# Kernel optimization log

Hardware: AMD Instinct MI355X
Metric: run time of the kernel (lower is better)

Reference implementation:

```python
import jax, jax.numpy as jnp
import numpy as np

B, N, S, K = 16, 4096, 1024, 32
DIN, DINC, DOUT = 64, 67, 64
MAX_VALUE = 1e10


def setup_inputs() -> dict:
    key = jax.random.key(0)
    ks = jax.random.split(key, 6)
    x = jax.random.normal(ks[0], (B, N, DIN), dtype=jnp.float32)
    x_complete = jax.random.normal(ks[1], (B, N, DINC), dtype=jnp.float32)
    # neighbor indices in [-1, N); -1 denotes padding (masked out in pooling)
    indexes = jax.random.randint(ks[2], (B, S, K), -1, N, dtype=jnp.int64)
    # first neighbor is the center point and must be valid
    indexes = indexes.at[:, :, 0].set(jnp.abs(indexes[:, :, 0]) % N)
    weight1 = jax.random.normal(ks[3], (DOUT, DINC), dtype=jnp.float32) * 0.05
    weight2 = jax.random.normal(ks[4], (DOUT, DIN), dtype=jnp.float32) * 0.05
    bias = jax.random.normal(ks[5], (DOUT,), dtype=jnp.float32) * 0.05
    return {"x": x, "x_complete": x_complete, "indexes": indexes,
            "weight1": weight1, "weight2": weight2, "bias": bias, "use_x": 1}


def reference(x, x_complete, indexes, weight1, weight2, bias, use_x):
    # pooling_operation = 'max' (hardcoded; string arg in original module)
    Bq, Nq, _ = x.shape
    _, Sq, Kq = indexes.shape
    C = weight1.shape[0]
    # dense linear projections
    xc = jnp.einsum('bnd,cd->bnc', x_complete, weight1) + bias  # (B,N,C)
    xp = jnp.einsum('bnd,cd->bnc', x, weight2)                  # (B,N,C)
    if use_x:
        xc = xc + xp
    # prepend a zero row so index -1 (-> slot 0) gathers zeros
    pad = jnp.concatenate([jnp.zeros((Bq, 1, C), xc.dtype), xc], axis=1)  # (B,N+1,C)
    idx1 = indexes + 1                                          # (B,S,K)
    g = jnp.take_along_axis(pad, idx1.reshape(Bq, Sq * Kq, 1), axis=1)
    g = g.reshape(Bq, Sq, Kq, C)                                # (B,S,K,C)
    if use_x:
        if Nq == Sq:
            g = g - xp[:, :, None, :]
        else:
            xp_pad = jnp.concatenate([jnp.zeros((Bq, 1, C), xp.dtype), xp], axis=1)
            center = jnp.take_along_axis(xp_pad, (indexes[:, :, 0] + 1)[:, :, None], axis=1)  # (B,S,C)
            g = g - center[:, :, None, :]
    # masked max over the neighbor axis: padded slots pushed to -MAX_VALUE
    mask = (idx1 == 0).astype(g.dtype)[..., None]               # (B,S,K,1)
    out = jnp.max(g - MAX_VALUE * mask, axis=2)                 # (B,S,C)
    return out
```

## Files before the change

### kernel.cpp

```cpp
#include <hip/hip_runtime.h>

#define B_    16
#define N_    4096
#define S_    1024
#define K_    32
#define DIN_  64
#define DINC_ 67
#define DOUT_ 64
#define ROWS_ (B_ * N_)
#define NCH   128
#define NFRAG 2560
#define ASTR  168

typedef float f32x4 __attribute__((ext_vector_type(4)));
typedef short s16x8 __attribute__((ext_vector_type(8)));

static __device__ __forceinline__ unsigned short f2bf(float f) {
    unsigned int u = __float_as_uint(f);
    u = (u + 0x7fffu + ((u >> 16) & 1u)) >> 16;
    return (unsigned short)u;
}
static __device__ __forceinline__ float bf2f(unsigned short h) {
    return __uint_as_float((unsigned int)h << 16);
}

__global__ __launch_bounds__(256) void prep_kernel(
    const float* __restrict__ w1, const float* __restrict__ w2,
    const int* __restrict__ use_x_p, uint4* __restrict__ wf)
{
    const int id = blockIdx.x * 256 + threadIdx.x;
    if (id >= NFRAG) return;
    const int s  = id >> 9;
    const int nt = (id >> 6) & 7;
    const int l  = id & 63;
    const int q  = l >> 4, m = l & 15;
    const int c  = nt * 16 + m;
    const int ux = use_x_p[0];

    unsigned int w[4];
#pragma unroll
    for (int p = 0; p < 4; ++p) {
        unsigned short h[2];
#pragma unroll
        for (int e = 0; e < 2; ++e) {
            const int j = p * 2 + e;
            const int k = s * 32 + q * 8 + j;
            float v = 0.f;
            if (c < 64) {
                if (k < DINC_)      v = w1[c * DINC_ + k];
                else if (k < 131)   v = ux ? w2[c * DIN_ + (k - DINC_)] : 0.f;
            } else {
                if (k >= DINC_ && k < 131) v = w2[(c - 64) * DIN_ + (k - DINC_)];
            }
            h[e] = f2bf(v);
        }
        w[p] = (unsigned int)h[0] | ((unsigned int)h[1] << 16);
    }
    wf[id] = make_uint4(w[0], w[1], w[2], w[3]);
}

__global__ __launch_bounds__(256) void proj_kernel(
    const float* __restrict__ x, const float* __restrict__ xcm,
    const uint4* __restrict__ wf, const float* __restrict__ bias,
    unsigned short* __restrict__ cmb)
{
    __shared__ uint4 ldsb[NFRAG];
    __shared__ unsigned short lact[64 * ASTR];

    const int t    = threadIdx.x;
    const int row0 = (blockIdx.x & 7) * (ROWS_ / 8) + (blockIdx.x >> 3) * 64;

    for (int i = t; i < NFRAG; i += 256) ldsb[i] = wf[i];

    {
        const float* sc = xcm + (size_t)row0 * DINC_;
        for (int i = t; i < 64 * DINC_; i += 256) {
            const int row = i / DINC_, d = i - row * DINC_;
            lact[row * ASTR + d] = f2bf(sc[i]);
        }
        const float* sx = x + (size_t)row0 * DIN_;
        for (int i = t; i < 64 * DIN_; i += 256)
            lact[(i >> 6) * ASTR + DINC_ + (i & 63)] = f2bf(sx[i]);
        for (int i = t; i < 64 * 29; i += 256) {
            const int row = i / 29, d = i - row * 29;
            lact[row * ASTR + 131 + d] = 0;
        }
    }
    __syncthreads();

    const int l = t & 63;
    const int w = __builtin_amdgcn_readfirstlane(t >> 6);
    const int q = l >> 4, m = l & 15;

    const unsigned short* arow = lact + (w * 16 + m) * ASTR;
    s16x8 af[5];
#pragma unroll
    for (int s = 0; s < 5; ++s)
        af[s] = *(const s16x8*)(arow + s * 32 + q * 8);

    const s16x8* bfr = (const s16x8*)ldsb;

    f32x4 acc[8];
#pragma unroll
    for (int nt = 0; nt < 8; ++nt) acc[nt] = (f32x4){0.f, 0.f, 0.f, 0.f};

#pragma unroll
    for (int s = 0; s < 5; ++s) {
#pragma unroll
        for (int nt = 0; nt < 8; ++nt) {
            const s16x8 bf = bfr[(s * 8 + nt) * 64 + l];
            acc[nt] = __builtin_amdgcn_mfma_f32_16x16x32_bf16(bf, af[s], acc[nt], 0, 0, 0);
        }
    }

    const int row_g = row0 + w * 16 + m;
    unsigned short* rowp = cmb + (size_t)row_g * NCH;
    const int chq = q * 4;
#pragma unroll
    for (int nt = 0; nt < 8; ++nt) {
        f32x4 a = acc[nt];
        if (nt < 4) {
            const float4 bv = *(const float4*)(bias + nt * 16 + chq);
            a[0] += bv.x; a[1] += bv.y; a[2] += bv.z; a[3] += bv.w;
        }
        const unsigned int lo = (unsigned int)f2bf(a[0]) | ((unsigned int)f2bf(a[1]) << 16);
        const unsigned int hi = (unsigned int)f2bf(a[2]) | ((unsigned int)f2bf(a[3]) << 16);
        *(uint2*)(rowp + nt * 16 + chq) = make_uint2(lo, hi);
    }
}

__global__ __launch_bounds__(256) void gather_max_kernel(
    const int* __restrict__ indexes, const unsigned short* __restrict__ cmb,
    const int* __restrict__ use_x_p, float* __restrict__ out)
{
    const int lane = threadIdx.x & 63;
    const int h    = lane >> 5;
    const int ln   = lane & 31;
    const int wv   = __builtin_amdgcn_readfirstlane(threadIdx.x >> 6);
    const int grp  = (blockIdx.x & 7) * 1024 + (blockIdx.x >> 3) * 4 + wv;
    const int pairA = grp * 2;
    const int b     = grp >> 9;
    const int ux    = use_x_p[0];

    const int* iA = indexes + (size_t)pairA * K_;
    const int* iB = iA + K_;
    const char* cb = (const char*)cmb + (size_t)b * N_ * 256;

    const float NEG = -__builtin_inff();
    float m0 = NEG, m1 = NEG;
#pragma unroll
    for (int k = 0; k < K_; ++k) {
        const int ia = iA[k], ib = iB[k];
        const int ik = h ? ib : ia;
        const int iku = ik < 0 ? 0 : ik;
        const unsigned int v = *(const unsigned int*)(cb + ((size_t)iku << 8) + ln * 4);
        const bool inv = ik < 0;
        m0 = fmaxf(m0, inv ? NEG : bf2f((unsigned short)(v & 0xffff)));
        m1 = fmaxf(m1, inv ? NEG : bf2f((unsigned short)(v >> 16)));
    }
    if (ux) {
        const int i0 = h ? iB[0] : iA[0];
        const unsigned int c = *(const unsigned int*)(cb + ((size_t)i0 << 8) + 128 + ln * 4);
        m0 -= bf2f((unsigned short)(c & 0xffff));
        m1 -= bf2f((unsigned short)(c >> 16));
    }
    const int pair = pairA + h;
    *(float2*)(out + (size_t)pair * 64 + ln * 2) = make_float2(m0, m1);
}

__global__ __launch_bounds__(256, 1) void fused_fallback_kernel(
    const float* __restrict__ x, const float* __restrict__ xcm,
    const int* __restrict__ indexes,
    const float* __restrict__ w1, const float* __restrict__ w2,
    const float* __restrict__ bias, const int* __restrict__ use_x_p,
    float* __restrict__ out)
{
    const int lane = threadIdx.x & 63;
    const int pair = (blockIdx.x * blockDim.x + threadIdx.x) >> 6;
    const int b    = pair >> 10;
    const int ux   = use_x_p[0];

    float W1[DINC_];
#pragma unroll
    for (int j = 0; j < DINC_; ++j) W1[j] = w1[lane * DINC_ + j];
    float W2[DIN_];
#pragma unroll
    for (int j = 0; j < DIN_; ++j) W2[j] = w2[lane * DIN_ + j];
    const float bv = bias[lane];

    const int* idxp  = indexes + (size_t)pair * K_;
    const int  myidx = idxp[lane & 31];

    const float NEG = -__builtin_inff();
    float m = NEG;
    for (int k = 0; k < K_; ++k) {
        const int ik = __shfl(myidx, k, 64);
        if (ik < 0) continue;
        const float* xc_row = xcm + ((size_t)b * N_ + ik) * DINC_;
        float a1 = bv;
#pragma unroll
        for (int j = 0; j < DINC_; ++j) a1 += xc_row[j] * W1[j];
        if (ux) {
            const float* x_row = x + ((size_t)b * N_ + ik) * DIN_;
            float a2 = 0.f;
#pragma unroll
            for (int j = 0; j < DIN_; ++j) a2 += x_row[j] * W2[j];
            a1 += a2;
        }
        m = fmaxf(m, a1);
    }
    if (ux) {
        const int i0 = __shfl(myidx, 0, 64);
        const float* x_row = x + ((size_t)b * N_ + i0) * DIN_;
        float a2 = 0.f;
#pragma unroll
        for (int j = 0; j < DIN_; ++j) a2 += x_row[j] * W2[j];
        m -= a2;
    }
    out[(size_t)pair * DOUT_ + lane] = m;
}

extern "C" void kernel_launch(void* const* d_in, const int* in_sizes, int n_in,
                              void* d_out, int out_size, void* d_ws, size_t ws_size,
                              hipStream_t stream)
{
    const float* x    = (const float*)d_in[0];
    const float* xcm  = (const float*)d_in[1];
    const int*   idx  = (const int*)d_in[2];
    const float* w1   = (const float*)d_in[3];
    const float* w2   = (const float*)d_in[4];
    const float* bias = (const float*)d_in[5];
    const int*   ux   = (const int*)d_in[6];
    float* out = (float*)d_out;

    const size_t cmb_bytes = (size_t)ROWS_ * NCH * sizeof(unsigned short);
    const size_t wf_bytes  = (size_t)NFRAG * 16;
    const int npairs = B_ * S_;

    if (ws_size >= cmb_bytes + wf_bytes) {
        unsigned short* cmb = (unsigned short*)d_ws;
        uint4* wf = (uint4*)((char*)d_ws + cmb_bytes);

        prep_kernel<<<(NFRAG + 255) / 256, 256, 0, stream>>>(w1, w2, ux, wf);
        proj_kernel<<<ROWS_ / 64, 256, 0, stream>>>(x, xcm, wf, bias, cmb);
        gather_max_kernel<<<(npairs / 2) / 4, 256, 0, stream>>>(idx, cmb, ux, out);
    } else {
        fused_fallback_kernel<<<npairs / 4, 256, 0, stream>>>(x, xcm, idx, w1, w2,
                                                              bias, ux, out);
    }
}
```

Baseline: 109.2 us.

## Reorder K layout to skip zero MFMA tiles and pack activation loads

The fused weight matrix's reduction axis is reordered so x comes first and x_complete second. The xp half of the output channels then only needs the first two K-slices, which cuts MFMA count from 40 to 28 per wave and shrinks the weight fragments held in LDS. The activation staging also reads float2 pairs and writes packed bf16 pairs as 32-bit LDS stores, replacing scalar 16-bit writes. The odd 67-wide x_complete rows use scalar loads, and the tail handling is more intricate.

```diff
diff --git a/kernel.cpp b/kernel.cpp
--- a/kernel.cpp
+++ b/kernel.cpp
@@ -9,8 +9,11 @@
 #define DOUT_ 64
 #define ROWS_ (B_ * N_)
 #define NCH   128
-#define NFRAG 2560
+#define NTILE 28
+#define NFRAG (NTILE * 64)
 #define ASTR  168
+#define WLDSB (NTILE * 64 * 16)
+#define ALDSB (64 * ASTR * 2)
 
 typedef float f32x4 __attribute__((ext_vector_type(4)));
 typedef short s16x8 __attribute__((ext_vector_type(8)));
@@ -23,6 +26,9 @@
 static __device__ __forceinline__ float bf2f(unsigned short h) {
     return __uint_as_float((unsigned int)h << 16);
 }
+static __device__ __forceinline__ unsigned int pack2(float a, float b) {
+    return (unsigned int)f2bf(a) | ((unsigned int)f2bf(b) << 16);
+}
 
 __global__ __launch_bounds__(256) void prep_kernel(
     const float* __restrict__ w1, const float* __restrict__ w2,
@@ -30,12 +36,13 @@
 {
     const int id = blockIdx.x * 256 + threadIdx.x;
     if (id >= NFRAG) return;
-    const int s  = id >> 9;
-    const int nt = (id >> 6) & 7;
-    const int l  = id & 63;
-    const int q  = l >> 4, m = l & 15;
-    const int c  = nt * 16 + m;
-    const int ux = use_x_p[0];
+    const int tile = id >> 6;
+    const int l    = id & 63;
+    const int s    = (tile < 16) ? (tile >> 3) : (2 + ((tile - 16) >> 2));
+    const int nt   = (tile < 16) ? (tile & 7)  : ((tile - 16) & 3);
+    const int q    = l >> 4, m = l & 15;
+    const int c    = nt * 16 + m;
+    const int ux   = use_x_p[0];
 
     unsigned int w[4];
 #pragma unroll
@@ -43,14 +50,13 @@
         unsigned short h[2];
 #pragma unroll
         for (int e = 0; e < 2; ++e) {
-            const int j = p * 2 + e;
-            const int k = s * 32 + q * 8 + j;
+            const int k = s * 32 + q * 8 + p * 2 + e;
             float v = 0.f;
             if (c < 64) {
-                if (k < DINC_)      v = w1[c * DINC_ + k];
-                else if (k < 131)   v = ux ? w2[c * DIN_ + (k - DINC_)] : 0.f;
+                if (k < 64)         v = ux ? w2[c * DIN_ + k] : 0.f;
+                else if (k < 131)   v = w1[c * DINC_ + (k - 64)];
             } else {
-                if (k >= DINC_ && k < 131) v = w2[(c - 64) * DIN_ + (k - DINC_)];
+                if (k < 64)         v = w2[(c - 64) * DIN_ + k];
             }
             h[e] = f2bf(v);
         }
@@ -64,8 +70,10 @@
     const uint4* __restrict__ wf, const float* __restrict__ bias,
     unsigned short* __restrict__ cmb)
 {
-    __shared__ uint4 ldsb[NFRAG];
-    __shared__ unsigned short lact[64 * ASTR];
+    __shared__ char smem[WLDSB + ALDSB];
+    uint4* ldsb          = (uint4*)smem;
+    unsigned short* lact = (unsigned short*)(smem + WLDSB);
+    unsigned int*  ldsd  = (unsigned int*)lact;
 
     const int t    = threadIdx.x;
     const int row0 = (blockIdx.x & 7) * (ROWS_ / 8) + (blockIdx.x >> 3) * 64;
@@ -73,17 +81,23 @@
     for (int i = t; i < NFRAG; i += 256) ldsb[i] = wf[i];
 
     {
+        const float* sx = x + (size_t)row0 * DIN_;
+        for (int i = t; i < 64 * 32; i += 256) {
+            const int row = i >> 5, d2 = i & 31;
+            const float2 v = *(const float2*)(sx + row * DIN_ + 2 * d2);
+            ldsd[row * 84 + d2] = pack2(v.x, v.y);
+        }
         const float* sc = xcm + (size_t)row0 * DINC_;
-        for (int i = t; i < 64 * DINC_; i += 256) {
-            const int row = i / DINC_, d = i - row * DINC_;
-            lact[row * ASTR + d] = f2bf(sc[i]);
-        }
-        const float* sx = x + (size_t)row0 * DIN_;
-        for (int i = t; i < 64 * DIN_; i += 256)
-            lact[(i >> 6) * ASTR + DINC_ + (i & 63)] = f2bf(sx[i]);
-        for (int i = t; i < 64 * 29; i += 256) {
-            const int row = i / 29, d = i - row * 29;
-            lact[row * ASTR + 131 + d] = 0;
+        for (int i = t; i < 64 * 33; i += 256) {
+            const int row = i / 33, j = i - row * 33;
+            const float a = sc[row * DINC_ + 2 * j];
+            const float b = sc[row * DINC_ + 2 * j + 1];
+            ldsd[row * 84 + 32 + j] = pack2(a, b);
+        }
+        for (int i = t; i < 64 * 15; i += 256) {
+            const int row = i / 15, j = i - row * 15;
+            ldsd[row * 84 + 65 + j] =
+                (j == 0) ? pack2(sc[row * DINC_ + 66], 0.f) : 0u;
         }
     }
     __syncthreads();
@@ -105,13 +119,17 @@
     for (int nt = 0; nt < 8; ++nt) acc[nt] = (f32x4){0.f, 0.f, 0.f, 0.f};
 
 #pragma unroll
-    for (int s = 0; s < 5; ++s) {
-#pragma unroll
-        for (int nt = 0; nt < 8; ++nt) {
-            const s16x8 bf = bfr[(s * 8 + nt) * 64 + l];
-            acc[nt] = __builtin_amdgcn_mfma_f32_16x16x32_bf16(bf, af[s], acc[nt], 0, 0, 0);
-        }
-    }
+    for (int s = 0; s < 2; ++s)
+#pragma unroll
+        for (int nt = 0; nt < 8; ++nt)
+            acc[nt] = __builtin_amdgcn_mfma_f32_16x16x32_bf16(
+                bfr[(s * 8 + nt) * 64 + l], af[s], acc[nt], 0, 0, 0);
+#pragma unroll
+    for (int s = 2; s < 5; ++s)
+#pragma unroll
+        for (int nt = 0; nt < 4; ++nt)
+            acc[nt] = __builtin_amdgcn_mfma_f32_16x16x32_bf16(
+                bfr[(16 + (s - 2) * 4 + nt) * 64 + l], af[s], acc[nt], 0, 0, 0);
 
     const int row_g = row0 + w * 16 + m;
     unsigned short* rowp = cmb + (size_t)row_g * NCH;
@@ -123,9 +141,8 @@
             const float4 bv = *(const float4*)(bias + nt * 16 + chq);
             a[0] += bv.x; a[1] += bv.y; a[2] += bv.z; a[3] += bv.w;
         }
-        const unsigned int lo = (unsigned int)f2bf(a[0]) | ((unsigned int)f2bf(a[1]) << 16);
-        const unsigned int hi = (unsigned int)f2bf(a[2]) | ((unsigned int)f2bf(a[3]) << 16);
-        *(uint2*)(rowp + nt * 16 + chq) = make_uint2(lo, hi);
+        *(uint2*)(rowp + nt * 16 + chq) =
+            make_uint2(pack2(a[0], a[1]), pack2(a[2], a[3]));
     }
 }
 
```

After: 112.6 us. 1.03x slower.
